# Performance work log

Hardware: AMD Instinct MI355X
Metric: run time of the kernel (lower is better)

Reference implementation:

```python
import jax, jax.numpy as jnp
import numpy as np
import math

INPUT_SIZE = 4096
NUM_NEURONS = 4096
ATTN_SIZE = 64
BATCH = 8192


def setup_inputs() -> dict:
    key = jax.random.key(0)
    ks = jax.random.split(key, 10)
    lim_in = 1.0 / math.sqrt(INPUT_SIZE)
    lim_a = 1.0 / math.sqrt(ATTN_SIZE)
    x = jax.random.normal(ks[0], (BATCH, INPUT_SIZE), dtype=jnp.float32)
    # attention linears (torch default uniform(-1/sqrt(fan_in), ...))
    Wq = jax.random.uniform(ks[1], (ATTN_SIZE, INPUT_SIZE), jnp.float32, -lim_in, lim_in)
    bq = jnp.zeros((ATTN_SIZE,), jnp.float32)
    Wk = jax.random.uniform(ks[2], (ATTN_SIZE, INPUT_SIZE), jnp.float32, -lim_in, lim_in)
    bk = jnp.zeros((ATTN_SIZE,), jnp.float32)
    Wv = jax.random.uniform(ks[3], (ATTN_SIZE, INPUT_SIZE), jnp.float32, -lim_in, lim_in)
    bv = jnp.zeros((ATTN_SIZE,), jnp.float32)
    Wo = jax.random.uniform(ks[4], (INPUT_SIZE, ATTN_SIZE), jnp.float32, -lim_a, lim_a)
    bo = jnp.zeros((INPUT_SIZE,), jnp.float32)
    # stacked single-weight neurons: weight ~ N(0,1)*0.01, bias 0
    Wn = jax.random.normal(ks[5], (NUM_NEURONS, INPUT_SIZE), jnp.float32) * 0.01
    bn = jnp.zeros((NUM_NEURONS,), jnp.float32)
    return {"x": x, "Wq": Wq, "bq": bq, "Wk": Wk, "bk": bk,
            "Wv": Wv, "bv": bv, "Wo": Wo, "bo": bo, "Wn": Wn, "bn": bn}


def reference(x, Wq, bq, Wk, bk, Wv, bv, Wo, bo, Wn, bn):
    scale = math.sqrt(ATTN_SIZE)
    # x is treated as a length-1 "sequence" of the full feature vector: [B, 1, S]
    q = x @ Wq.T + bq            # [B, A]
    k = x @ Wk.T + bk            # [B, A]
    v = x @ Wv.T + bv            # [B, A]
    # attention over a single token: softmax of a single score == 1, kept for fidelity
    scores = jnp.sum(q * k, axis=-1, keepdims=True) / scale      # [B, 1]
    attn_w = jax.nn.softmax(scores[:, :, None], axis=-1)          # [B, 1, 1] -> all ones
    attended = attn_w[:, 0, :] * v                                # [B, A] == v
    attn_out = attended @ Wo.T + bo                               # [B, S]
    h = attn_out + x                                              # residual
    # stacked single-weight neurons == one GEMM
    out = h @ Wn.T + bn                                           # [B, N]
    return jax.nn.relu(out)
```

## Files before the change

### kernel.cpp

```cpp
#include <hip/hip_runtime.h>
#include <stdint.h>


typedef unsigned short u16;
typedef float f32x4 __attribute__((ext_vector_type(4)));
typedef __bf16 bf16x8 __attribute__((ext_vector_type(8)));
typedef u16 u16x8 __attribute__((ext_vector_type(8)));

__device__ __forceinline__ float b2f(u16 u) {
  union { unsigned int i; float f; } x; x.i = ((unsigned int)u) << 16; return x.f;
}
__device__ __forceinline__ u16 f2b(float f) {
  union { float f; unsigned int i; } x; x.f = f;
  unsigned int r = x.i + 0x7FFFu + ((x.i >> 16) & 1u);
  return (u16)(r >> 16);
}

__device__ __forceinline__ void gl_lds16(const u16* g, u16* l) {
#if __has_builtin(__builtin_amdgcn_global_load_lds)
  __builtin_amdgcn_global_load_lds((__attribute__((address_space(1))) void*)g,
                                   (__attribute__((address_space(3))) void*)l, 16, 0, 0);
#else
  int lane = threadIdx.x & 63;
  *(u16x8*)(l + lane * 8) = *(const u16x8*)g;
#endif
}

__device__ __forceinline__ f32x4 mfma16(bf16x8 a, bf16x8 b, f32x4 c) {
  return __builtin_amdgcn_mfma_f32_16x16x32_bf16(a, b, c, 0, 0, 0);
}

#define XCH 4194304L
#define WNCH 2097152L
#define WVCH 32768L
__global__ __launch_bounds__(256) void k_cvt(
    const float* __restrict__ x, const float* __restrict__ Wn, const float* __restrict__ Wv,
    u16* __restrict__ xb, u16* __restrict__ Wnb, u16* __restrict__ Wvb) {
  long i = (long)blockIdx.x * 256 + threadIdx.x;
  const float* src; u16* dst; long off;
  if (i < XCH) { src = x; dst = xb; off = i * 8; }
  else if (i < XCH + WNCH) { src = Wn; dst = Wnb; off = (i - XCH) * 8; }
  else { src = Wv; dst = Wvb; off = (i - XCH - WNCH) * 8; }
  f32x4 a = *(const f32x4*)&src[off];
  f32x4 b = *(const f32x4*)&src[off + 4];
  u16x8 o;
#pragma unroll
  for (int e = 0; e < 4; ++e) { o[e] = f2b(a[e]); o[4 + e] = f2b(b[e]); }
  *(u16x8*)&dst[off] = o;
}

__global__ __launch_bounds__(256) void kT(const float* __restrict__ Wo, u16* __restrict__ WoT) {
  __shared__ __align__(16) u16 t[64 * 72];
  const int b = blockIdx.x;
  const int tid = threadIdx.x;
  {
    int k = tid >> 2, a0 = (tid & 3) * 16;
    const float* src = &Wo[(size_t)(b * 64 + k) * 64 + a0];
#pragma unroll
    for (int q = 0; q < 4; ++q) {
      f32x4 v = *(const f32x4*)&src[q * 4];
#pragma unroll
      for (int e = 0; e < 4; ++e) t[k * 72 + a0 + q * 4 + e] = f2b(v[e]);
    }
  }
  __syncthreads();
  {
    int a = tid >> 2, k0 = (tid & 3) * 16;
    u16x8 o0, o1;
#pragma unroll
    for (int j = 0; j < 8; ++j) o0[j] = t[(k0 + j) * 72 + a];
#pragma unroll
    for (int j = 0; j < 8; ++j) o1[j] = t[(k0 + 8 + j) * 72 + a];
    *(u16x8*)&WoT[(size_t)a * 4096 + b * 64 + k0] = o0;
    *(u16x8*)&WoT[(size_t)a * 4096 + b * 64 + k0 + 8] = o1;
  }
}

#define PBK 128
__device__ void gemm_n64(const u16* __restrict__ A, const u16* __restrict__ B,
                         u16* __restrict__ C, const float* __restrict__ bias,
                         long m0, u16* lA, u16* lB) {
  const int tid = threadIdx.x;
  const int w = tid >> 6, l = tid & 63;
  f32x4 acc[4];
#pragma unroll
  for (int nt = 0; nt < 4; ++nt) acc[nt] = (f32x4)(0.f);

  for (int k0 = 0; k0 < 4096; k0 += PBK) {
    __syncthreads();
#pragma unroll
    for (int i = 0; i < 4; ++i) {
      int row = w * 16 + i * 4 + (l >> 4);
      int p = (l & 15) ^ (i * 4 + (l >> 4));
      gl_lds16(A + (m0 + row) * (long)4096 + k0 + p * 8, lA + (w * 16 + i * 4) * PBK);
      gl_lds16(B + (long)row * 4096 + k0 + p * 8, lB + (w * 16 + i * 4) * PBK);
    }
    __syncthreads();
#pragma unroll
    for (int kk = 0; kk < 4; ++kk) {
      int slotA = ((kk * 4 + (l >> 4)) ^ (l & 15)) * 8;
      bf16x8 af = *(const bf16x8*)&lA[(w * 16 + (l & 15)) * PBK + slotA];
#pragma unroll
      for (int nt = 0; nt < 4; ++nt) {
        bf16x8 bf = *(const bf16x8*)&lB[(nt * 16 + (l & 15)) * PBK + slotA];
        acc[nt] = mfma16(af, bf, acc[nt]);
      }
    }
  }
#pragma unroll
  for (int nt = 0; nt < 4; ++nt) {
    int col = nt * 16 + (l & 15);
    float bb = bias ? bias[col] : 0.f;
#pragma unroll
    for (int r = 0; r < 4; ++r) {
      long row = m0 + w * 16 + (l >> 4) * 4 + r;
      C[row * 64 + col] = f2b(acc[nt][r] + bb);
    }
  }
}

__global__ __launch_bounds__(256, 2) void k_prep(
    const u16* __restrict__ xb, const u16* __restrict__ Wvb, const float* __restrict__ bv,
    const u16* __restrict__ Wnb, const u16* __restrict__ WoT,
    const float* __restrict__ bo, const float* __restrict__ bn,
    u16* __restrict__ V, u16* __restrict__ Wm, float* __restrict__ biasTot) {
  __shared__ __align__(16) u16 lA[64 * PBK];
  __shared__ __align__(16) u16 lB[64 * PBK];
  const int bid = blockIdx.x;
  if (bid < 128) {
    gemm_n64(xb, Wvb, V, bv, (long)bid * 64, lA, lB);
  } else if (bid < 192) {
    gemm_n64(Wnb, WoT, Wm, nullptr, (long)(bid - 128) * 64, lA, lB);
  } else {
    const int w = threadIdx.x >> 6, l = threadIdx.x & 63;
    const int n = (bid - 192) * 4 + w;
    float s = 0.f;
#pragma unroll
    for (int j = 0; j < 8; ++j) {
      int off = (j * 64 + l) * 8;
      u16x8 a = *(const u16x8*)&Wnb[(size_t)n * 4096 + off];
      f32x4 c0 = *(const f32x4*)&bo[off];
      f32x4 c1 = *(const f32x4*)&bo[off + 4];
#pragma unroll
      for (int e = 0; e < 4; ++e) s += b2f(a[e]) * c0[e] + b2f(a[4 + e]) * c1[e];
    }
#pragma unroll
    for (int o = 32; o > 0; o >>= 1) s += __shfl_xor(s, o, 64);
    if (l == 0) biasTot[n] = s + bn[n];
  }
}

__global__ __launch_bounds__(256, 2) void k_main(
    const u16* __restrict__ X, const u16* __restrict__ Wn,
    const u16* __restrict__ V, const u16* __restrict__ Wm,
    const float* __restrict__ biasTot, float* __restrict__ Out) {
  __shared__ __align__(16) u16 smem[2 * 128 * 32];
  u16* lA = smem;
  u16* lB = smem + 128 * 32;
  const int tid = threadIdx.x;
  const int w = tid >> 6, l = tid & 63;
  const int wRow = (w & 1) * 64, wCol = (w >> 1) * 64;
  const long mBase = (long)(blockIdx.x >> 5) * 128;
  const int nBase = (int)(blockIdx.x & 31) * 128;

  f32x4 acc[4][4];
#pragma unroll
  for (int mt = 0; mt < 4; ++mt)
#pragma unroll
    for (int nt = 0; nt < 4; ++nt) acc[mt][nt] = (f32x4)(0.f);

  const int rl = l >> 2;
  const int kp = (l & 3) * 8;

  for (int k0 = 0; k0 < 4096; k0 += 32) {
    __syncthreads();
#pragma unroll
    for (int i = 0; i < 2; ++i) {
      int row = w * 32 + i * 16 + rl;
      gl_lds16(X + (mBase + row) * (long)4096 + k0 + kp, lA + (w * 32 + i * 16) * 32);
      gl_lds16(Wn + (long)(nBase + row) * 4096 + k0 + kp, lB + (w * 32 + i * 16) * 32);
    }
    __syncthreads();
    bf16x8 af[4], bfr[4];
#pragma unroll
    for (int mt = 0; mt < 4; ++mt)
      af[mt] = *(const bf16x8*)&lA[(wRow + mt * 16 + (l & 15)) * 32 + (l >> 4) * 8];
#pragma unroll
    for (int nt = 0; nt < 4; ++nt)
      bfr[nt] = *(const bf16x8*)&lB[(wCol + nt * 16 + (l & 15)) * 32 + (l >> 4) * 8];
#pragma unroll
    for (int mt = 0; mt < 4; ++mt)
#pragma unroll
      for (int nt = 0; nt < 4; ++nt) acc[mt][nt] = mfma16(af[mt], bfr[nt], acc[mt][nt]);
  }

  for (int k0 = 0; k0 < 64; k0 += 32) {
    __syncthreads();
#pragma unroll
    for (int i = 0; i < 2; ++i) {
      int row = w * 32 + i * 16 + rl;
      gl_lds16(V + (mBase + row) * (long)64 + k0 + kp, lA + (w * 32 + i * 16) * 32);
      gl_lds16(Wm + (long)(nBase + row) * 64 + k0 + kp, lB + (w * 32 + i * 16) * 32);
    }
    __syncthreads();
    bf16x8 af[4], bfr[4];
#pragma unroll
    for (int mt = 0; mt < 4; ++mt)
      af[mt] = *(const bf16x8*)&lA[(wRow + mt * 16 + (l & 15)) * 32 + (l >> 4) * 8];
#pragma unroll
    for (int nt = 0; nt < 4; ++nt)
      bfr[nt] = *(const bf16x8*)&lB[(wCol + nt * 16 + (l & 15)) * 32 + (l >> 4) * 8];
#pragma unroll
    for (int mt = 0; mt < 4; ++mt)
#pragma unroll
      for (int nt = 0; nt < 4; ++nt) acc[mt][nt] = mfma16(af[mt], bfr[nt], acc[mt][nt]);
  }

  __syncthreads();
  float* eb = ((float*)smem) + w * 1024;
#pragma unroll
  for (int mt = 0; mt < 4; ++mt) {
#pragma unroll
    for (int nt = 0; nt < 4; ++nt) {
      float bt = biasTot[nBase + wCol + nt * 16 + (l & 15)];
#pragma unroll
      for (int r = 0; r < 4; ++r) {
        float val = acc[mt][nt][r] + bt;
        eb[((l >> 4) * 4 + r) * 64 + nt * 16 + (l & 15)] = fmaxf(val, 0.f);
      }
    }
    int rr = l >> 2, c0 = (l & 3) * 16;
    long grow = mBase + wRow + mt * 16 + rr;
    int gcol = nBase + wCol + c0;
    f32x4 o0 = *(const f32x4*)&eb[rr * 64 + c0];
    f32x4 o1 = *(const f32x4*)&eb[rr * 64 + c0 + 4];
    f32x4 o2 = *(const f32x4*)&eb[rr * 64 + c0 + 8];
    f32x4 o3 = *(const f32x4*)&eb[rr * 64 + c0 + 12];
    *(f32x4*)&Out[grow * 4096 + gcol] = o0;
    *(f32x4*)&Out[grow * 4096 + gcol + 4] = o1;
    *(f32x4*)&Out[grow * 4096 + gcol + 8] = o2;
    *(f32x4*)&Out[grow * 4096 + gcol + 12] = o3;
  }
}

extern "C" void kernel_launch(void* const* d_in, const int* in_sizes, int n_in,
                              void* d_out, int out_size, void* d_ws, size_t ws_size,
                              hipStream_t stream) {
  const float* x  = (const float*)d_in[0];
  const float* Wv = (const float*)d_in[5];
  const float* bv = (const float*)d_in[6];
  const float* Wo = (const float*)d_in[7];
  const float* bo = (const float*)d_in[8];
  const float* Wn = (const float*)d_in[9];
  const float* bn = (const float*)d_in[10];
  float* out = (float*)d_out;

  char* ws = (char*)d_ws;
  u16* xb  = (u16*)ws;
  u16* Wnb = (u16*)(ws + (64L << 20));
  u16* Wvb = (u16*)(ws + (96L << 20));
  u16* WoT = (u16*)(ws + (96L << 20) + (512 << 10));
  u16* V   = (u16*)(ws + (97L << 20));
  u16* Wm  = (u16*)(ws + (98L << 20));
  float* biasTot = (float*)(ws + (98L << 20) + (512 << 10));

  k_cvt<<<dim3(24704), dim3(256), 0, stream>>>(x, Wn, Wv, xb, Wnb, Wvb);
  kT<<<dim3(64), dim3(256), 0, stream>>>(Wo, WoT);
  k_prep<<<dim3(1216), dim3(256), 0, stream>>>(xb, Wvb, bv, Wnb, WoT, bo, bn, V, Wm, biasTot);
  k_main<<<dim3(2048), dim3(256), 0, stream>>>(xb, Wnb, V, Wm, biasTot, out);
}
```

Measured before the change: 666.3 us.

## Fuse conversion, transpose and prep GEMMs into one preprocessing kernel

Replaces the separate conversion, Wo transpose and prep kernels with a single k_pre launch. It converts x to bf16 inside the V GEMM, computes Wm = Wn·Wo and the bias totals with fp32 scalar dot products straight from the fp32 inputs, and converts Wn in separate blocks. This removes two launches, the intermediate Wvb/WoT buffers and one pass re-reading bf16 x. The trade is that the Wm path now does slow scalar fp32 work and reads Wn twice (once for Wm, once for conversion), and V blocks now handle only 32 rows each.

```diff
diff --git a/kernel.cpp b/kernel.cpp
--- a/kernel.cpp
+++ b/kernel.cpp
@@ -30,123 +30,122 @@
   return __builtin_amdgcn_mfma_f32_16x16x32_bf16(a, b, c, 0, 0, 0);
 }
 
-#define XCH 4194304L
-#define WNCH 2097152L
-#define WVCH 32768L
-__global__ __launch_bounds__(256) void k_cvt(
-    const float* __restrict__ x, const float* __restrict__ Wn, const float* __restrict__ Wv,
-    u16* __restrict__ xb, u16* __restrict__ Wnb, u16* __restrict__ Wvb) {
-  long i = (long)blockIdx.x * 256 + threadIdx.x;
-  const float* src; u16* dst; long off;
-  if (i < XCH) { src = x; dst = xb; off = i * 8; }
-  else if (i < XCH + WNCH) { src = Wn; dst = Wnb; off = (i - XCH) * 8; }
-  else { src = Wv; dst = Wvb; off = (i - XCH - WNCH) * 8; }
-  f32x4 a = *(const f32x4*)&src[off];
-  f32x4 b = *(const f32x4*)&src[off + 4];
-  u16x8 o;
-#pragma unroll
-  for (int e = 0; e < 4; ++e) { o[e] = f2b(a[e]); o[4 + e] = f2b(b[e]); }
-  *(u16x8*)&dst[off] = o;
-}
-
-__global__ __launch_bounds__(256) void kT(const float* __restrict__ Wo, u16* __restrict__ WoT) {
-  __shared__ __align__(16) u16 t[64 * 72];
-  const int b = blockIdx.x;
+#define LDAP 136
+__global__ __launch_bounds__(256, 2) void k_pre(
+    const float* __restrict__ x, const float* __restrict__ Wv, const float* __restrict__ bv,
+    const float* __restrict__ Wo, const float* __restrict__ bo,
+    const float* __restrict__ Wn, const float* __restrict__ bn,
+    u16* __restrict__ xb, u16* __restrict__ Wnb,
+    u16* __restrict__ V, u16* __restrict__ Wm, float* __restrict__ biasTot) {
+  __shared__ __align__(16) u16 smem[32 * LDAP + 64 * LDAP];
+  const int bid = blockIdx.x;
   const int tid = threadIdx.x;
-  {
-    int k = tid >> 2, a0 = (tid & 3) * 16;
-    const float* src = &Wo[(size_t)(b * 64 + k) * 64 + a0];
-#pragma unroll
-    for (int q = 0; q < 4; ++q) {
-      f32x4 v = *(const f32x4*)&src[q * 4];
-#pragma unroll
-      for (int e = 0; e < 4; ++e) t[k * 72 + a0 + q * 4 + e] = f2b(v[e]);
-    }
-  }
-  __syncthreads();
-  {
-    int a = tid >> 2, k0 = (tid & 3) * 16;
-    u16x8 o0, o1;
-#pragma unroll
-    for (int j = 0; j < 8; ++j) o0[j] = t[(k0 + j) * 72 + a];
-#pragma unroll
-    for (int j = 0; j < 8; ++j) o1[j] = t[(k0 + 8 + j) * 72 + a];
-    *(u16x8*)&WoT[(size_t)a * 4096 + b * 64 + k0] = o0;
-    *(u16x8*)&WoT[(size_t)a * 4096 + b * 64 + k0 + 8] = o1;
-  }
-}
-
-#define PBK 128
-__device__ void gemm_n64(const u16* __restrict__ A, const u16* __restrict__ B,
-                         u16* __restrict__ C, const float* __restrict__ bias,
-                         long m0, u16* lA, u16* lB) {
-  const int tid = threadIdx.x;
+
+  if (bid >= 768) {
+    long off = ((long)(bid - 768) * 256 + tid) * 8;
+    f32x4 a = *(const f32x4*)&Wn[off];
+    f32x4 b = *(const f32x4*)&Wn[off + 4];
+    u16x8 o;
+#pragma unroll
+    for (int e = 0; e < 4; ++e) { o[e] = f2b(a[e]); o[4 + e] = f2b(b[e]); }
+    *(u16x8*)&Wnb[off] = o;
+    return;
+  }
+
+  if (bid >= 256) {
+    const long m0 = (long)(bid - 256) * 8;
+    const int r = tid >> 6, a = tid & 63;
+    const long row0 = m0 + r, row1 = m0 + 4 + r;
+    const float* wn0p = &Wn[row0 * 4096];
+    const float* wn1p = &Wn[row1 * 4096];
+    float acc0 = 0.f, acc1 = 0.f;
+    for (int k0 = 0; k0 < 4096; k0 += 8) {
+      f32x4 a0 = *(const f32x4*)&wn0p[k0];
+      f32x4 a1 = *(const f32x4*)&wn0p[k0 + 4];
+      f32x4 b0 = *(const f32x4*)&wn1p[k0];
+      f32x4 b1 = *(const f32x4*)&wn1p[k0 + 4];
+      float wo[8];
+#pragma unroll
+      for (int j = 0; j < 8; ++j) wo[j] = Wo[(long)(k0 + j) * 64 + a];
+#pragma unroll
+      for (int j = 0; j < 4; ++j) { acc0 += a0[j] * wo[j]; acc1 += b0[j] * wo[j]; }
+#pragma unroll
+      for (int j = 0; j < 4; ++j) { acc0 += a1[j] * wo[4 + j]; acc1 += b1[j] * wo[4 + j]; }
+    }
+    Wm[row0 * 64 + a] = f2b(acc0);
+    Wm[row1 * 64 + a] = f2b(acc1);
+    float p0 = 0.f, p1 = 0.f;
+#pragma unroll 4
+    for (int j = 0; j < 64; ++j) {
+      float bb = bo[j * 64 + a];
+      p0 += wn0p[j * 64 + a] * bb;
+      p1 += wn1p[j * 64 + a] * bb;
+    }
+#pragma unroll
+    for (int o = 32; o > 0; o >>= 1) { p0 += __shfl_xor(p0, o, 64); p1 += __shfl_xor(p1, o, 64); }
+    if (a == 0) { biasTot[row0] = p0 + bn[row0]; biasTot[row1] = p1 + bn[row1]; }
+    return;
+  }
+
   const int w = tid >> 6, l = tid & 63;
-  f32x4 acc[4];
-#pragma unroll
-  for (int nt = 0; nt < 4; ++nt) acc[nt] = (f32x4)(0.f);
-
-  for (int k0 = 0; k0 < 4096; k0 += PBK) {
-    __syncthreads();
-#pragma unroll
-    for (int i = 0; i < 4; ++i) {
-      int row = w * 16 + i * 4 + (l >> 4);
-      int p = (l & 15) ^ (i * 4 + (l >> 4));
-      gl_lds16(A + (m0 + row) * (long)4096 + k0 + p * 8, lA + (w * 16 + i * 4) * PBK);
-      gl_lds16(B + (long)row * 4096 + k0 + p * 8, lB + (w * 16 + i * 4) * PBK);
+  u16* lA = smem;
+  u16* lB = smem + 32 * LDAP;
+  const long m0 = (long)bid * 32;
+  const int mt = (w & 1) * 16, nb = (w >> 1) * 32;
+  f32x4 acc[2];
+  acc[0] = (f32x4)(0.f); acc[1] = (f32x4)(0.f);
+
+  for (int k0 = 0; k0 < 4096; k0 += 128) {
+    __syncthreads();
+    {
+      int row = tid >> 3, c0 = (tid & 7) * 16;
+      const float* s = &x[(m0 + row) * 4096 + k0 + c0];
+      u16* gxb = &xb[(m0 + row) * 4096 + k0 + c0];
+#pragma unroll
+      for (int q = 0; q < 2; ++q) {
+        f32x4 v0 = *(const f32x4*)&s[q * 8];
+        f32x4 v1 = *(const f32x4*)&s[q * 8 + 4];
+        u16x8 o;
+#pragma unroll
+        for (int e = 0; e < 4; ++e) { o[e] = f2b(v0[e]); o[4 + e] = f2b(v1[e]); }
+        *(u16x8*)&lA[row * LDAP + c0 + q * 8] = o;
+        *(u16x8*)&gxb[q * 8] = o;
+      }
+    }
+    {
+      int row = tid >> 2, c0 = (tid & 3) * 32;
+      const float* s = &Wv[(long)row * 4096 + k0 + c0];
+#pragma unroll
+      for (int q = 0; q < 4; ++q) {
+        f32x4 v0 = *(const f32x4*)&s[q * 8];
+        f32x4 v1 = *(const f32x4*)&s[q * 8 + 4];
+        u16x8 o;
+#pragma unroll
+        for (int e = 0; e < 4; ++e) { o[e] = f2b(v0[e]); o[4 + e] = f2b(v1[e]); }
+        *(u16x8*)&lB[row * LDAP + c0 + q * 8] = o;
+      }
     }
     __syncthreads();
 #pragma unroll
     for (int kk = 0; kk < 4; ++kk) {
-      int slotA = ((kk * 4 + (l >> 4)) ^ (l & 15)) * 8;
-      bf16x8 af = *(const bf16x8*)&lA[(w * 16 + (l & 15)) * PBK + slotA];
-#pragma unroll
-      for (int nt = 0; nt < 4; ++nt) {
-        bf16x8 bf = *(const bf16x8*)&lB[(nt * 16 + (l & 15)) * PBK + slotA];
+      int ko = kk * 32 + (l >> 4) * 8;
+      bf16x8 af = *(const bf16x8*)&lA[(mt + (l & 15)) * LDAP + ko];
+#pragma unroll
+      for (int nt = 0; nt < 2; ++nt) {
+        bf16x8 bf = *(const bf16x8*)&lB[(nb + nt * 16 + (l & 15)) * LDAP + ko];
         acc[nt] = mfma16(af, bf, acc[nt]);
       }
     }
   }
 #pragma unroll
-  for (int nt = 0; nt < 4; ++nt) {
-    int col = nt * 16 + (l & 15);
-    float bb = bias ? bias[col] : 0.f;
-#pragma unroll
-    for (int r = 0; r < 4; ++r) {
-      long row = m0 + w * 16 + (l >> 4) * 4 + r;
-      C[row * 64 + col] = f2b(acc[nt][r] + bb);
-    }
-  }
-}
-
-__global__ __launch_bounds__(256, 2) void k_prep(
-    const u16* __restrict__ xb, const u16* __restrict__ Wvb, const float* __restrict__ bv,
-    const u16* __restrict__ Wnb, const u16* __restrict__ WoT,
-    const float* __restrict__ bo, const float* __restrict__ bn,
-    u16* __restrict__ V, u16* __restrict__ Wm, float* __restrict__ biasTot) {
-  __shared__ __align__(16) u16 lA[64 * PBK];
-  __shared__ __align__(16) u16 lB[64 * PBK];
-  const int bid = blockIdx.x;
-  if (bid < 128) {
-    gemm_n64(xb, Wvb, V, bv, (long)bid * 64, lA, lB);
-  } else if (bid < 192) {
-    gemm_n64(Wnb, WoT, Wm, nullptr, (long)(bid - 128) * 64, lA, lB);
-  } else {
-    const int w = threadIdx.x >> 6, l = threadIdx.x & 63;
-    const int n = (bid - 192) * 4 + w;
-    float s = 0.f;
-#pragma unroll
-    for (int j = 0; j < 8; ++j) {
-      int off = (j * 64 + l) * 8;
-      u16x8 a = *(const u16x8*)&Wnb[(size_t)n * 4096 + off];
-      f32x4 c0 = *(const f32x4*)&bo[off];
-      f32x4 c1 = *(const f32x4*)&bo[off + 4];
-#pragma unroll
-      for (int e = 0; e < 4; ++e) s += b2f(a[e]) * c0[e] + b2f(a[4 + e]) * c1[e];
-    }
-#pragma unroll
-    for (int o = 32; o > 0; o >>= 1) s += __shfl_xor(s, o, 64);
-    if (l == 0) biasTot[n] = s + bn[n];
+  for (int nt = 0; nt < 2; ++nt) {
+    int col = nb + nt * 16 + (l & 15);
+    float bb = bv[col];
+#pragma unroll
+    for (int r2 = 0; r2 < 4; ++r2) {
+      long row = m0 + mt + (l >> 4) * 4 + r2;
+      V[row * 64 + col] = f2b(acc[nt][r2] + bb);
+    }
   }
 }
 
@@ -258,14 +257,11 @@
   char* ws = (char*)d_ws;
   u16* xb  = (u16*)ws;
   u16* Wnb = (u16*)(ws + (64L << 20));
-  u16* Wvb = (u16*)(ws + (96L << 20));
-  u16* WoT = (u16*)(ws + (96L << 20) + (512 << 10));
-  u16* V   = (u16*)(ws + (97L << 20));
-  u16* Wm  = (u16*)(ws + (98L << 20));
-  float* biasTot = (float*)(ws + (98L << 20) + (512 << 10));
-
-  k_cvt<<<dim3(24704), dim3(256), 0, stream>>>(x, Wn, Wv, xb, Wnb, Wvb);
-  kT<<<dim3(64), dim3(256), 0, stream>>>(Wo, WoT);
-  k_prep<<<dim3(1216), dim3(256), 0, stream>>>(xb, Wvb, bv, Wnb, WoT, bo, bn, V, Wm, biasTot);
+  u16* V   = (u16*)(ws + (96L << 20));
+  u16* Wm  = (u16*)(ws + (97L << 20));
+  float* biasTot = (float*)(ws + (97L << 20) + (512 << 10));
+
+  k_pre<<<dim3(8960), dim3(256), 0, stream>>>(x, Wv, bv, Wo, bo, Wn, bn,
+                                              xb, Wnb, V, Wm, biasTot);
   k_main<<<dim3(2048), dim3(256), 0, stream>>>(xb, Wnb, V, Wm, biasTot, out);
 }
```

After: 804.9 us. 20.8% more time.

## Double K tile to 64 with XOR-swizzled LDS layout and merged loops

Applied to the files above, without the earlier changes.

The main GEMM loop now stages a 64-wide K slice per iteration instead of 32, halving the number of barrier pairs. The LDS layout uses an XOR swizzle on 16-byte chunks so fragment reads avoid bank conflicts. The small V·Wm tail GEMM is folded into the same loop as its 65th iteration. This doubles LDS use per block and adds swizzle index math and a per-iteration branch.

```diff
diff --git a/kernel.cpp b/kernel.cpp
--- a/kernel.cpp
+++ b/kernel.cpp
@@ -32,7 +32,6 @@
 
 #define XCH 4194304L
 #define WNCH 2097152L
-#define WVCH 32768L
 __global__ __launch_bounds__(256) void k_cvt(
     const float* __restrict__ x, const float* __restrict__ Wn, const float* __restrict__ Wv,
     u16* __restrict__ xb, u16* __restrict__ Wnb, u16* __restrict__ Wvb) {
@@ -154,9 +153,9 @@
     const u16* __restrict__ X, const u16* __restrict__ Wn,
     const u16* __restrict__ V, const u16* __restrict__ Wm,
     const float* __restrict__ biasTot, float* __restrict__ Out) {
-  __shared__ __align__(16) u16 smem[2 * 128 * 32];
+  __shared__ __align__(16) u16 smem[2 * 128 * 64];
   u16* lA = smem;
-  u16* lB = smem + 128 * 32;
+  u16* lB = smem + 128 * 64;
   const int tid = threadIdx.x;
   const int w = tid >> 6, l = tid & 63;
   const int wRow = (w & 1) * 64, wCol = (w >> 1) * 64;
@@ -169,51 +168,36 @@
 #pragma unroll
     for (int nt = 0; nt < 4; ++nt) acc[mt][nt] = (f32x4)(0.f);
 
-  const int rl = l >> 2;
-  const int kp = (l & 3) * 8;
-
-  for (int k0 = 0; k0 < 4096; k0 += 32) {
-    __syncthreads();
-#pragma unroll
-    for (int i = 0; i < 2; ++i) {
-      int row = w * 32 + i * 16 + rl;
-      gl_lds16(X + (mBase + row) * (long)4096 + k0 + kp, lA + (w * 32 + i * 16) * 32);
-      gl_lds16(Wn + (long)(nBase + row) * 4096 + k0 + kp, lB + (w * 32 + i * 16) * 32);
-    }
-    __syncthreads();
-    bf16x8 af[4], bfr[4];
-#pragma unroll
-    for (int mt = 0; mt < 4; ++mt)
-      af[mt] = *(const bf16x8*)&lA[(wRow + mt * 16 + (l & 15)) * 32 + (l >> 4) * 8];
-#pragma unroll
-    for (int nt = 0; nt < 4; ++nt)
-      bfr[nt] = *(const bf16x8*)&lB[(wCol + nt * 16 + (l & 15)) * 32 + (l >> 4) * 8];
-#pragma unroll
-    for (int mt = 0; mt < 4; ++mt)
-#pragma unroll
-      for (int nt = 0; nt < 4; ++nt) acc[mt][nt] = mfma16(af[mt], bfr[nt], acc[mt][nt]);
-  }
-
-  for (int k0 = 0; k0 < 64; k0 += 32) {
-    __syncthreads();
-#pragma unroll
-    for (int i = 0; i < 2; ++i) {
-      int row = w * 32 + i * 16 + rl;
-      gl_lds16(V + (mBase + row) * (long)64 + k0 + kp, lA + (w * 32 + i * 16) * 32);
-      gl_lds16(Wm + (long)(nBase + row) * 64 + k0 + kp, lB + (w * 32 + i * 16) * 32);
-    }
-    __syncthreads();
-    bf16x8 af[4], bfr[4];
-#pragma unroll
-    for (int mt = 0; mt < 4; ++mt)
-      af[mt] = *(const bf16x8*)&lA[(wRow + mt * 16 + (l & 15)) * 32 + (l >> 4) * 8];
-#pragma unroll
-    for (int nt = 0; nt < 4; ++nt)
-      bfr[nt] = *(const bf16x8*)&lB[(wCol + nt * 16 + (l & 15)) * 32 + (l >> 4) * 8];
-#pragma unroll
-    for (int mt = 0; mt < 4; ++mt)
-#pragma unroll
-      for (int nt = 0; nt < 4; ++nt) acc[mt][nt] = mfma16(af[mt], bfr[nt], acc[mt][nt]);
+  const int srow = l >> 3;
+  const int sp = ((l & 7) ^ srow) * 8;
+
+  for (int kb = 0; kb < 65; ++kb) {
+    const u16 *pA, *pB; long lda;
+    if (kb < 64) { pA = X + (long)kb * 64; pB = Wn + (long)kb * 64; lda = 4096; }
+    else         { pA = V;                 pB = Wm;                 lda = 64;  }
+    __syncthreads();
+#pragma unroll
+    for (int i = 0; i < 4; ++i) {
+      int row = w * 32 + i * 8 + srow;
+      gl_lds16(pA + (mBase + row) * lda + sp, lA + (w * 32 + i * 8) * 64);
+      gl_lds16(pB + (long)(nBase + row) * lda + sp, lB + (w * 32 + i * 8) * 64);
+    }
+    __syncthreads();
+#pragma unroll
+    for (int kk = 0; kk < 2; ++kk) {
+      int slot = ((kk * 4 + (l >> 4)) ^ (l & 7)) * 8;
+      bf16x8 af[4], bfr[4];
+#pragma unroll
+      for (int mt = 0; mt < 4; ++mt)
+        af[mt] = *(const bf16x8*)&lA[(wRow + mt * 16 + (l & 15)) * 64 + slot];
+#pragma unroll
+      for (int nt = 0; nt < 4; ++nt)
+        bfr[nt] = *(const bf16x8*)&lB[(wCol + nt * 16 + (l & 15)) * 64 + slot];
+#pragma unroll
+      for (int mt = 0; mt < 4; ++mt)
+#pragma unroll
+        for (int nt = 0; nt < 4; ++nt) acc[mt][nt] = mfma16(af[mt], bfr[nt], acc[mt][nt]);
+    }
   }
 
   __syncthreads();
```

Result: faster. 605.9 us (-9.1%).
